# Optimization experiments

Hardware: AMD Instinct MI355X
Metric: run time of the kernel (lower is better)

The kernel has to match this reference:

```python
import jax, jax.numpy as jnp
import numpy as np

N = 4_000_000
IN_H, OUT_H = 4, 4
DIMS = [IN_H, 8, 16, 32, 16, 8, OUT_H]


def setup_inputs() -> dict:
    key = jax.random.key(0)
    keys = jax.random.split(key, 2 * len(DIMS))
    inp = {"x": jax.random.normal(keys[0], (N, IN_H), dtype=jnp.float32)}
    for i in range(6):
        fan_in, fan_out = DIMS[i], DIMS[i + 1]
        bound = 1.0 / np.sqrt(fan_in)
        # torch nn.Linear default init: U(-1/sqrt(fan_in), 1/sqrt(fan_in))
        inp[f"W{i+1}"] = jax.random.uniform(keys[2 * i + 1], (fan_in, fan_out),
                                             minval=-bound, maxval=bound, dtype=jnp.float32)
        inp[f"b{i+1}"] = jax.random.uniform(keys[2 * i + 2], (fan_out,),
                                             minval=-bound, maxval=bound, dtype=jnp.float32)
    return inp


def reference(x, W1, b1, W2, b2, W3, b3, W4, b4, W5, b5, W6, b6):
    # Six Linear+ReLU pairs, ReLU after every layer including the last.
    h = x
    for W, b in ((W1, b1), (W2, b2), (W3, b3), (W4, b4), (W5, b5), (W6, b6)):
        h = jax.nn.relu(h @ W + b)
    return h
```

## Files before the change

### kernel.cpp

```cpp
#include <hip/hip_runtime.h>


typedef _Float16 f16x8 __attribute__((ext_vector_type(8)));
typedef float    f32x16 __attribute__((ext_vector_type(16)));
typedef unsigned int u32;
typedef u32 u32x4v __attribute__((ext_vector_type(4)));

#define DEV __device__ __forceinline__

DEV u32 pk(float a, float b) {
  return __builtin_bit_cast(u32, __builtin_amdgcn_cvt_pkrtz(a, b));
}
DEV u32 pkr(float a, float b) {
  u32 p = pk(a, b), r;
  asm("v_pk_max_f16 %0, %1, 0" : "=v"(r) : "v"(p));
  return r;
}
DEV void swap32(u32& a, u32& b) {
  asm("v_permlane32_swap_b32 %0, %1" : "+v"(a), "+v"(b));
}
DEV f16x8 mkB(u32 a, u32 b, u32 c, u32 d) {
  u32x4v v = {a, b, c, d};
  return __builtin_bit_cast(f16x8, v);
}

DEV f16x8 wfragT32(const float* __restrict__ W, int IN, int ld, int mvalid,
                   int koff, const float* __restrict__ bias, int kbias,
                   int lane) {
  const int m  = lane & 31;
  const int k0 = (lane >> 5) * 8;
  f16x8 r = {0, 0, 0, 0, 0, 0, 0, 0};
#pragma unroll
  for (int j = 0; j < 8; ++j) {
    const int kg = koff + k0 + j;
    float w = 0.0f;
    if (m < mvalid) {
      if (kg < IN)            w = W[kg * ld + m];
      else if (bias && kg == kbias) w = bias[m];
    }
    r[j] = (_Float16)w;
  }
  return r;
}

DEV f32x16 biasC32(const float* __restrict__ b, int nvalid, int lane) {
  const int H = lane >> 5;
  f32x16 c;
#pragma unroll
  for (int r = 0; r < 16; ++r) {
    const int m = (r & 3) + 8 * (r >> 2) + 4 * H;
    c[r] = (m < nvalid) ? b[m] : 0.0f;
  }
  return c;
}

#define MFMA32(A, B, C) __builtin_amdgcn_mfma_f32_32x32x16_f16((A), (B), (C), 0, 0, 0)

__global__ void __launch_bounds__(256)
mlp6_mfma32(const float* __restrict__ x,
            const float* __restrict__ W1, const float* __restrict__ b1,
            const float* __restrict__ W2, const float* __restrict__ b2,
            const float* __restrict__ W3, const float* __restrict__ b3,
            const float* __restrict__ W4, const float* __restrict__ b4,
            const float* __restrict__ W5, const float* __restrict__ b5,
            const float* __restrict__ W6, const float* __restrict__ b6,
            float* __restrict__ out, int nchunks) {
  const int  lane = threadIdx.x & 63;
  const bool hi32 = lane >= 32;

  const f16x8 A1  = wfragT32(W1, 4, 8, 8, 0, b1, 4, lane);
  const f16x8 A2  = wfragT32(W2, 8, 16, 16, 0, b2, 8, lane);
  const f16x8 A3  = wfragT32(W3, 16, 32, 32, 0, nullptr, -1, lane);
  const f16x8 A4a = wfragT32(W4, 32, 16, 16, 0, nullptr, -1, lane);
  const f16x8 A4b = wfragT32(W4, 32, 16, 16, 16, nullptr, -1, lane);
  const f16x8 A5  = wfragT32(W5, 16, 8, 8, 0, nullptr, -1, lane);
  const f16x8 A6  = wfragT32(W6, 8, 4, 4, 0, b6, 8, lane);

  const f32x16 C3 = biasC32(b3, 32, lane);
  const f32x16 C4 = biasC32(b4, 16, lane);
  const f32x16 C5 = biasC32(b5, 8, lane);
  const f32x16 Z  = {};

  const u32 kone = 0x00003C00u;

  const int gw = (int)((blockIdx.x * blockDim.x + threadIdx.x) >> 6);
  const int nw = (int)((gridDim.x * blockDim.x) >> 6);

  for (int ch = gw; ch < nchunks; ch += nw) {
    const size_t base = (size_t)ch * 64;

    const float4 xr = *reinterpret_cast<const float4*>(x + (base + lane) * 4);
    const u32 xp0 = pk(xr.x, xr.y);
    const u32 xp1 = pk(xr.z, xr.w);

#pragma unroll
    for (int t = 0; t < 2; ++t) {
      u32 i0 = xp0, i1 = xp1;
      if (t == 1) {
        u32 c0 = xp0, c1 = xp0; swap32(c0, c1);
        u32 c2 = xp1, c3 = xp1; swap32(c2, c3);
        i0 = c1; i1 = c3;
      }
      f32x16 D = MFMA32(A1, mkB(i0, i1, kone, kone), Z);

      u32 q0 = pkr(D[0], D[1]);
      u32 q1 = pkr(D[2], D[3]);
      u32 c0 = q0, c1 = q0; swap32(c0, c1);
      u32 c2 = q1, c3 = q1; swap32(c2, c3);
      u32 dw0 = hi32 ? kone : q0;
      D = MFMA32(A2, mkB(dw0, q1, c1, c3), Z);

      q0 = pkr(D[0], D[1]); q1 = pkr(D[2], D[3]);
      u32 q2 = pkr(D[4], D[5]); u32 q3 = pkr(D[6], D[7]);
      swap32(q0, q2);
      swap32(q1, q3);
      D = MFMA32(A3, mkB(q0, q1, q2, q3), C3);

      u32 r0 = pkr(D[0], D[1]),  r1 = pkr(D[2], D[3]);
      u32 r2 = pkr(D[4], D[5]),  r3 = pkr(D[6], D[7]);
      u32 r4 = pkr(D[8], D[9]),  r5 = pkr(D[10], D[11]);
      u32 r6 = pkr(D[12], D[13]), r7 = pkr(D[14], D[15]);
      swap32(r0, r2); swap32(r1, r3);
      swap32(r4, r6); swap32(r5, r7);
      D = MFMA32(A4a, mkB(r0, r1, r2, r3), C4);
      D = MFMA32(A4b, mkB(r4, r5, r6, r7), D);

      q0 = pkr(D[0], D[1]); q1 = pkr(D[2], D[3]);
      q2 = pkr(D[4], D[5]); q3 = pkr(D[6], D[7]);
      swap32(q0, q2); swap32(q1, q3);
      D = MFMA32(A5, mkB(q0, q1, q2, q3), C5);

      q0 = pkr(D[0], D[1]); q1 = pkr(D[2], D[3]);
      c0 = q0; c1 = q0; swap32(c0, c1);
      c2 = q1; c3 = q1; swap32(c2, c3);
      dw0 = hi32 ? kone : q0;
      D = MFMA32(A6, mkB(dw0, q1, c1, c3), Z);

      if (!hi32) {
        const float4 o = make_float4(fmaxf(D[0], 0.0f), fmaxf(D[1], 0.0f),
                                     fmaxf(D[2], 0.0f), fmaxf(D[3], 0.0f));
        *reinterpret_cast<float4*>(out + (base + (size_t)t * 32 + lane) * 4) = o;
      }
    }
  }
}

extern "C" void kernel_launch(void* const* d_in, const int* in_sizes, int n_in,
                              void* d_out, int out_size, void* d_ws, size_t ws_size,
                              hipStream_t stream) {
  const float* x  = (const float*)d_in[0];
  const float* W1 = (const float*)d_in[1];
  const float* b1 = (const float*)d_in[2];
  const float* W2 = (const float*)d_in[3];
  const float* b2 = (const float*)d_in[4];
  const float* W3 = (const float*)d_in[5];
  const float* b3 = (const float*)d_in[6];
  const float* W4 = (const float*)d_in[7];
  const float* b4 = (const float*)d_in[8];
  const float* W5 = (const float*)d_in[9];
  const float* b5 = (const float*)d_in[10];
  const float* W6 = (const float*)d_in[11];
  const float* b6 = (const float*)d_in[12];
  float* out = (float*)d_out;

  const int nrows   = in_sizes[0] / 4;
  const int nchunks = nrows / 64;

  mlp6_mfma32<<<dim3(2048), dim3(256), 0, stream>>>(
      x, W1, b1, W2, b2, W3, b3, W4, b4, W5, b5, W6, b6, out, nchunks);
}
```

Baseline: 192.9 us.

## Interleave two MFMA chains, prefetch next chunk, fold biases into packed f16 adds

Runs the two 32-row halves of each 64-row chunk as independent interleaved MFMA dependency chains instead of serially, so the MFMA latencies of one half can hide behind the other. Prefetches the next chunk's input during the current computation. Replaces the fp32 bias accumulator initialization with packed f16 bias adds after conversion, which frees accumulator registers but rounds the bias to f16. Halves the grid to 1024 blocks. The cost is higher register pressure and slightly different numerics.

```diff
diff --git a/kernel.cpp b/kernel.cpp
--- a/kernel.cpp
+++ b/kernel.cpp
@@ -11,10 +11,26 @@
 DEV u32 pk(float a, float b) {
   return __builtin_bit_cast(u32, __builtin_amdgcn_cvt_pkrtz(a, b));
 }
-DEV u32 pkr(float a, float b) {
-  u32 p = pk(a, b), r;
+DEV u32 pk_rne(float a, float b) {
+  const u32 ra = (u32)__builtin_bit_cast(unsigned short, (_Float16)a);
+  const u32 rb = (u32)__builtin_bit_cast(unsigned short, (_Float16)b);
+  return ra | (rb << 16);
+}
+DEV u32 pkmax0(u32 p) {
+  u32 r;
   asm("v_pk_max_f16 %0, %1, 0" : "=v"(r) : "v"(p));
   return r;
+}
+DEV u32 pkadd(u32 a, u32 b) {
+  u32 r;
+  asm("v_pk_add_f16 %0, %1, %2" : "=v"(r) : "v"(a), "v"(b));
+  return r;
+}
+DEV u32 pkr(float a, float b) {
+  return pkmax0(pk(a, b));
+}
+DEV u32 pkrb(float a, float b, u32 pbias) {
+  return pkmax0(pkadd(pk(a, b), pbias));
 }
 DEV void swap32(u32& a, u32& b) {
   asm("v_permlane32_swap_b32 %0, %1" : "+v"(a), "+v"(b));
@@ -35,7 +51,7 @@
     const int kg = koff + k0 + j;
     float w = 0.0f;
     if (m < mvalid) {
-      if (kg < IN)            w = W[kg * ld + m];
+      if (kg < IN)                  w = W[kg * ld + m];
       else if (bias && kg == kbias) w = bias[m];
     }
     r[j] = (_Float16)w;
@@ -43,30 +59,20 @@
   return r;
 }
 
-DEV f32x16 biasC32(const float* __restrict__ b, int nvalid, int lane) {
-  const int H = lane >> 5;
-  f32x16 c;
-#pragma unroll
-  for (int r = 0; r < 16; ++r) {
-    const int m = (r & 3) + 8 * (r >> 2) + 4 * H;
-    c[r] = (m < nvalid) ? b[m] : 0.0f;
-  }
-  return c;
-}
-
 #define MFMA32(A, B, C) __builtin_amdgcn_mfma_f32_32x32x16_f16((A), (B), (C), 0, 0, 0)
 
 __global__ void __launch_bounds__(256)
-mlp6_mfma32(const float* __restrict__ x,
-            const float* __restrict__ W1, const float* __restrict__ b1,
-            const float* __restrict__ W2, const float* __restrict__ b2,
-            const float* __restrict__ W3, const float* __restrict__ b3,
-            const float* __restrict__ W4, const float* __restrict__ b4,
-            const float* __restrict__ W5, const float* __restrict__ b5,
-            const float* __restrict__ W6, const float* __restrict__ b6,
-            float* __restrict__ out, int nchunks) {
+mlp6_ilv(const float* __restrict__ x,
+         const float* __restrict__ W1, const float* __restrict__ b1,
+         const float* __restrict__ W2, const float* __restrict__ b2,
+         const float* __restrict__ W3, const float* __restrict__ b3,
+         const float* __restrict__ W4, const float* __restrict__ b4,
+         const float* __restrict__ W5, const float* __restrict__ b5,
+         const float* __restrict__ W6, const float* __restrict__ b6,
+         float* __restrict__ out, int nchunks) {
   const int  lane = threadIdx.x & 63;
   const bool hi32 = lane >= 32;
+  const int  H    = lane >> 5;
 
   const f16x8 A1  = wfragT32(W1, 4, 8, 8, 0, b1, 4, lane);
   const f16x8 A2  = wfragT32(W2, 8, 16, 16, 0, b2, 8, lane);
@@ -76,72 +82,131 @@
   const f16x8 A5  = wfragT32(W5, 16, 8, 8, 0, nullptr, -1, lane);
   const f16x8 A6  = wfragT32(W6, 8, 4, 4, 0, b6, 8, lane);
 
-  const f32x16 C3 = biasC32(b3, 32, lane);
-  const f32x16 C4 = biasC32(b4, 16, lane);
-  const f32x16 C5 = biasC32(b5, 8, lane);
-  const f32x16 Z  = {};
-
+  u32 pb3[8], pb4[4], pb5[2];
+#pragma unroll
+  for (int i = 0; i < 8; ++i) {
+    const int m0 = ((2 * i) & 3) + 8 * ((2 * i) >> 2) + 4 * H;
+    pb3[i] = pk_rne(b3[m0], b3[m0 + 1]);
+  }
+#pragma unroll
+  for (int i = 0; i < 4; ++i) {
+    const int m0 = ((2 * i) & 3) + 8 * ((2 * i) >> 2) + 4 * H;
+    pb4[i] = pk_rne(b4[m0], b4[m0 + 1]);
+  }
+#pragma unroll
+  for (int i = 0; i < 2; ++i) {
+    const int m0 = ((2 * i) & 3) + 4 * H;
+    pb5[i] = pk_rne(b5[m0], b5[m0 + 1]);
+  }
+
+  const f32x16 Z = {};
   const u32 kone = 0x00003C00u;
 
   const int gw = (int)((blockIdx.x * blockDim.x + threadIdx.x) >> 6);
   const int nw = (int)((gridDim.x * blockDim.x) >> 6);
 
+  if (gw >= nchunks) return;
+
+  float4 xr = *reinterpret_cast<const float4*>(x + ((size_t)gw * 64 + lane) * 4);
+
   for (int ch = gw; ch < nchunks; ch += nw) {
     const size_t base = (size_t)ch * 64;
-
-    const float4 xr = *reinterpret_cast<const float4*>(x + (base + lane) * 4);
+    const int nxt = (ch + nw < nchunks) ? ch + nw : ch;
+    const float4 xn =
+        *reinterpret_cast<const float4*>(x + ((size_t)nxt * 64 + lane) * 4);
+
     const u32 xp0 = pk(xr.x, xr.y);
     const u32 xp1 = pk(xr.z, xr.w);
 
-#pragma unroll
-    for (int t = 0; t < 2; ++t) {
-      u32 i0 = xp0, i1 = xp1;
-      if (t == 1) {
-        u32 c0 = xp0, c1 = xp0; swap32(c0, c1);
-        u32 c2 = xp1, c3 = xp1; swap32(c2, c3);
-        i0 = c1; i1 = c3;
-      }
-      f32x16 D = MFMA32(A1, mkB(i0, i1, kone, kone), Z);
-
-      u32 q0 = pkr(D[0], D[1]);
-      u32 q1 = pkr(D[2], D[3]);
-      u32 c0 = q0, c1 = q0; swap32(c0, c1);
-      u32 c2 = q1, c3 = q1; swap32(c2, c3);
-      u32 dw0 = hi32 ? kone : q0;
-      D = MFMA32(A2, mkB(dw0, q1, c1, c3), Z);
-
-      q0 = pkr(D[0], D[1]); q1 = pkr(D[2], D[3]);
-      u32 q2 = pkr(D[4], D[5]); u32 q3 = pkr(D[6], D[7]);
-      swap32(q0, q2);
-      swap32(q1, q3);
-      D = MFMA32(A3, mkB(q0, q1, q2, q3), C3);
-
-      u32 r0 = pkr(D[0], D[1]),  r1 = pkr(D[2], D[3]);
-      u32 r2 = pkr(D[4], D[5]),  r3 = pkr(D[6], D[7]);
-      u32 r4 = pkr(D[8], D[9]),  r5 = pkr(D[10], D[11]);
-      u32 r6 = pkr(D[12], D[13]), r7 = pkr(D[14], D[15]);
+    u32 i00 = xp0, i10 = xp0; swap32(i00, i10);
+    u32 i01 = xp1, i11 = xp1; swap32(i01, i11);
+
+    f32x16 D0 = MFMA32(A1, mkB(i00, i01, kone, kone), Z);
+    f32x16 D1 = MFMA32(A1, mkB(i10, i11, kone, kone), Z);
+
+    {
+      u32 q0 = pkr(D0[0], D0[1]), q1 = pkr(D0[2], D0[3]);
+      u32 c0 = q0, c1 = q0; swap32(c0, c1);
+      u32 c2 = q1, c3 = q1; swap32(c2, c3);
+      D0 = MFMA32(A2, mkB(hi32 ? kone : q0, q1, c1, c3), Z);
+    }
+    {
+      u32 q0 = pkr(D1[0], D1[1]), q1 = pkr(D1[2], D1[3]);
+      u32 c0 = q0, c1 = q0; swap32(c0, c1);
+      u32 c2 = q1, c3 = q1; swap32(c2, c3);
+      D1 = MFMA32(A2, mkB(hi32 ? kone : q0, q1, c1, c3), Z);
+    }
+
+    {
+      u32 q0 = pkr(D0[0], D0[1]), q1 = pkr(D0[2], D0[3]);
+      u32 q2 = pkr(D0[4], D0[5]), q3 = pkr(D0[6], D0[7]);
+      swap32(q0, q2); swap32(q1, q3);
+      D0 = MFMA32(A3, mkB(q0, q1, q2, q3), Z);
+    }
+    {
+      u32 q0 = pkr(D1[0], D1[1]), q1 = pkr(D1[2], D1[3]);
+      u32 q2 = pkr(D1[4], D1[5]), q3 = pkr(D1[6], D1[7]);
+      swap32(q0, q2); swap32(q1, q3);
+      D1 = MFMA32(A3, mkB(q0, q1, q2, q3), Z);
+    }
+
+    {
+      u32 r0 = pkrb(D0[0], D0[1], pb3[0]),  r1 = pkrb(D0[2], D0[3], pb3[1]);
+      u32 r2 = pkrb(D0[4], D0[5], pb3[2]),  r3 = pkrb(D0[6], D0[7], pb3[3]);
+      u32 r4 = pkrb(D0[8], D0[9], pb3[4]),  r5 = pkrb(D0[10], D0[11], pb3[5]);
+      u32 r6 = pkrb(D0[12], D0[13], pb3[6]), r7 = pkrb(D0[14], D0[15], pb3[7]);
       swap32(r0, r2); swap32(r1, r3);
       swap32(r4, r6); swap32(r5, r7);
-      D = MFMA32(A4a, mkB(r0, r1, r2, r3), C4);
-      D = MFMA32(A4b, mkB(r4, r5, r6, r7), D);
-
-      q0 = pkr(D[0], D[1]); q1 = pkr(D[2], D[3]);
-      q2 = pkr(D[4], D[5]); q3 = pkr(D[6], D[7]);
-      swap32(q0, q2); swap32(q1, q3);
-      D = MFMA32(A5, mkB(q0, q1, q2, q3), C5);
-
-      q0 = pkr(D[0], D[1]); q1 = pkr(D[2], D[3]);
-      c0 = q0; c1 = q0; swap32(c0, c1);
-      c2 = q1; c3 = q1; swap32(c2, c3);
-      dw0 = hi32 ? kone : q0;
-      D = MFMA32(A6, mkB(dw0, q1, c1, c3), Z);
-
-      if (!hi32) {
-        const float4 o = make_float4(fmaxf(D[0], 0.0f), fmaxf(D[1], 0.0f),
-                                     fmaxf(D[2], 0.0f), fmaxf(D[3], 0.0f));
-        *reinterpret_cast<float4*>(out + (base + (size_t)t * 32 + lane) * 4) = o;
-      }
-    }
+      D0 = MFMA32(A4a, mkB(r0, r1, r2, r3), Z);
+      D0 = MFMA32(A4b, mkB(r4, r5, r6, r7), D0);
+    }
+    {
+      u32 r0 = pkrb(D1[0], D1[1], pb3[0]),  r1 = pkrb(D1[2], D1[3], pb3[1]);
+      u32 r2 = pkrb(D1[4], D1[5], pb3[2]),  r3 = pkrb(D1[6], D1[7], pb3[3]);
+      u32 r4 = pkrb(D1[8], D1[9], pb3[4]),  r5 = pkrb(D1[10], D1[11], pb3[5]);
+      u32 r6 = pkrb(D1[12], D1[13], pb3[6]), r7 = pkrb(D1[14], D1[15], pb3[7]);
+      swap32(r0, r2); swap32(r1, r3);
+      swap32(r4, r6); swap32(r5, r7);
+      D1 = MFMA32(A4a, mkB(r0, r1, r2, r3), Z);
+      D1 = MFMA32(A4b, mkB(r4, r5, r6, r7), D1);
+    }
+
+    {
+      u32 q0 = pkrb(D0[0], D0[1], pb4[0]), q1 = pkrb(D0[2], D0[3], pb4[1]);
+      u32 q2 = pkrb(D0[4], D0[5], pb4[2]), q3 = pkrb(D0[6], D0[7], pb4[3]);
+      swap32(q0, q2); swap32(q1, q3);
+      D0 = MFMA32(A5, mkB(q0, q1, q2, q3), Z);
+    }
+    {
+      u32 q0 = pkrb(D1[0], D1[1], pb4[0]), q1 = pkrb(D1[2], D1[3], pb4[1]);
+      u32 q2 = pkrb(D1[4], D1[5], pb4[2]), q3 = pkrb(D1[6], D1[7], pb4[3]);
+      swap32(q0, q2); swap32(q1, q3);
+      D1 = MFMA32(A5, mkB(q0, q1, q2, q3), Z);
+    }
+
+    {
+      u32 q0 = pkrb(D0[0], D0[1], pb5[0]), q1 = pkrb(D0[2], D0[3], pb5[1]);
+      u32 c0 = q0, c1 = q0; swap32(c0, c1);
+      u32 c2 = q1, c3 = q1; swap32(c2, c3);
+      D0 = MFMA32(A6, mkB(hi32 ? kone : q0, q1, c1, c3), Z);
+    }
+    {
+      u32 q0 = pkrb(D1[0], D1[1], pb5[0]), q1 = pkrb(D1[2], D1[3], pb5[1]);
+      u32 c0 = q0, c1 = q0; swap32(c0, c1);
+      u32 c2 = q1, c3 = q1; swap32(c2, c3);
+      D1 = MFMA32(A6, mkB(hi32 ? kone : q0, q1, c1, c3), Z);
+    }
+
+    if (!hi32) {
+      const float4 o0 = make_float4(fmaxf(D0[0], 0.0f), fmaxf(D0[1], 0.0f),
+                                    fmaxf(D0[2], 0.0f), fmaxf(D0[3], 0.0f));
+      *reinterpret_cast<float4*>(out + (base + lane) * 4) = o0;
+      const float4 o1 = make_float4(fmaxf(D1[0], 0.0f), fmaxf(D1[1], 0.0f),
+                                    fmaxf(D1[2], 0.0f), fmaxf(D1[3], 0.0f));
+      *reinterpret_cast<float4*>(out + (base + 32 + lane) * 4) = o1;
+    }
+
+    xr = xn;
   }
 }
 
@@ -166,6 +231,6 @@
   const int nrows   = in_sizes[0] / 4;
   const int nchunks = nrows / 64;
 
-  mlp6_mfma32<<<dim3(2048), dim3(256), 0, stream>>>(
+  mlp6_ilv<<<dim3(1024), dim3(256), 0, stream>>>(
       x, W1, b1, W2, b2, W3, b3, W4, b4, W5, b5, W6, b6, out, nchunks);
 }
```

Result: faster. 166.1 us (-13.9%).
